# Optimization experiments

Hardware: AMD Instinct MI355X
Metric: run time of the kernel (lower is better)

The kernel has to match this reference:

```python
import jax, jax.numpy as jnp
import numpy as np

MAX_SH_DEGREE = 3
NUM_BASES = (MAX_SH_DEGREE + 1) ** 2  # 16


def eval_sh_bases_fast(dirs):
    """SH bases up to degree 3 for unit directions [..., 3] -> [..., 16].
    Matches gsplat's _eval_sh_bases_fast constants/order."""
    x, y, z = dirs[..., 0], dirs[..., 1], dirs[..., 2]
    z2 = z * z
    fTmp0B = -1.092548430592079 * z
    fC1 = x * x - y * y
    fS1 = 2.0 * x * y
    fTmp0C = -2.285228997322329 * z2 + 0.4570457994644658
    fTmp1B = 1.445305721320277 * z
    fC2 = x * fC1 - y * fS1
    fS2 = x * fS1 + y * fC1
    ones = jnp.full_like(x, 0.2820947917738781)
    return jnp.stack([
        ones,
        -0.48860251190292 * y,
        0.48860251190292 * z,
        -0.48860251190292 * x,
        0.5462742152960395 * fS1,
        fTmp0B * y,
        0.9461746957575601 * z2 - 0.3153915652525201,
        fTmp0B * x,
        0.5462742152960395 * fC1,
        -0.5900435899266435 * fS2,
        fTmp1B * fS1,
        fTmp0C * y,
        z * (1.865881662950577 * z2 - 1.119528997770346),
        fTmp0C * x,
        fTmp1B * fC1,
        -0.5900435899266435 * fC2,
    ], axis=-1)


def setup_inputs() -> dict:
    key = jax.random.key(0)
    ks = jax.random.split(key, 10)
    C, N, F, E, W = 4, 250000, 32, 16, 128
    D_IN = E + F + NUM_BASES  # 64
    return {
        "features": jax.random.normal(ks[0], (N, F), jnp.float32),
        "dirs": jax.random.normal(ks[1], (C, N, 3), jnp.float32),
        "embed_table": jax.random.normal(ks[2], (1000, E), jnp.float32) * 0.1,
        "W0": jax.random.normal(ks[3], (D_IN, W), jnp.float32) / np.sqrt(D_IN),
        "b0": jax.random.normal(ks[4], (W,), jnp.float32) * 0.01,
        "W1": jax.random.normal(ks[5], (W, W), jnp.float32) / np.sqrt(W),
        "b1": jax.random.normal(ks[6], (W,), jnp.float32) * 0.01,
        "W2": jax.random.normal(ks[7], (W, 3), jnp.float32) / np.sqrt(W),
        "b2": jax.random.normal(ks[8], (3,), jnp.float32) * 0.01,
        "embed_ids": jax.random.randint(ks[9], (C,), 0, 1000, jnp.int64 if jax.config.jax_enable_x64 else jnp.int32),
        "sh_degree": 3,
    }


def reference(features, dirs, embed_table, W0, b0, W1, b1, W2, b2, embed_ids, sh_degree):
    C, N = dirs.shape[:2]
    E = embed_table.shape[1]
    F_dim = features.shape[1]
    # camera embeddings broadcast over splats
    emb = embed_table[embed_ids]                                   # [C, E]
    emb = jnp.broadcast_to(emb[:, None, :], (C, N, E))
    feats = jnp.broadcast_to(features[None, :, :], (C, N, F_dim))
    # F.normalize(dirs, dim=-1): divide by norm clamped at eps=1e-12
    norm = jnp.linalg.norm(dirs, axis=-1, keepdims=True)
    nd = dirs / jnp.maximum(norm, 1e-12)
    nb_use = (sh_degree + 1) ** 2  # static python int
    sh = eval_sh_bases_fast(nd)                                    # [C, N, 16]
    if nb_use < NUM_BASES:  # zero bases beyond requested degree
        mask = (jnp.arange(NUM_BASES) < nb_use).astype(sh.dtype)
        sh = sh * mask
    x = jnp.concatenate([emb, feats, sh], axis=-1)                 # [C, N, 64]
    h = jax.nn.relu(x @ W0 + b0)
    h = jax.nn.relu(h @ W1 + b1)
    return h @ W2 + b2                                             # [C, N, 3]
```

## Files before the change

### kernel.cpp

```cpp
#include <hip/hip_runtime.h>
#include <cstdint>
#include <cstddef>

typedef _Float16 half8 __attribute__((ext_vector_type(8)));
typedef __fp16 fp16x2 __attribute__((ext_vector_type(2)));
typedef float floatx16 __attribute__((ext_vector_type(16)));


__global__ void vdc_prep_kernel(const float* __restrict__ W0,
                                const float* __restrict__ W1,
                                const float* __restrict__ W2,
                                const float* __restrict__ b0,
                                const float* __restrict__ b1,
                                const float* __restrict__ b2,
                                const float* __restrict__ emb_tab,
                                const int* __restrict__ embed_ids,
                                int C,
                                _Float16* __restrict__ ws) {
    int i = blockIdx.x * 256 + threadIdx.x;
    int w0end = C * 8192;
    int w1end = w0end + 18432;
    int w2end = w1end + 4608;
    float v = 0.0f;
    if (i < w0end) {
        int c = i >> 13, r = i & 8191;
        int ci = r >> 9, l = (r >> 3) & 63, ii = r & 7;
        int mt = ci >> 2, ks = ci & 3;
        int j  = mt * 32 + (l & 31);
        int kk = ks * 16 + (l >> 5) * 8 + ii;
        if (kk < 48) v = W0[(16 + kk) * 128 + j];
        else if (kk == 48) {
            int id = embed_ids[c];
            v = b0[j];
            #pragma unroll
            for (int e = 0; e < 16; ++e)
                v += emb_tab[(size_t)id * 16 + e] * W0[e * 128 + j];
        }
        ws[i] = (_Float16)v;
    } else if (i < w1end) {
        int r = i - w0end;
        int ci = r >> 9, l = (r >> 3) & 63, ii = r & 7;
        int mt = ci / 9, ks = ci - mt * 9;
        int j  = mt * 32 + (l & 31);
        int kk = ks * 16 + (l >> 5) * 8 + ii;
        if (kk < 128) v = W1[kk * 128 + j];
        else if (kk == 128) v = b1[j];
        ws[i] = (_Float16)v;
    } else if (i < w2end) {
        int r = i - w1end;
        int ks = r >> 9, l = (r >> 3) & 63, ii = r & 7;
        int o  = l & 31;
        int kk = ks * 16 + (l >> 5) * 8 + ii;
        if (o < 3) {
            if (kk < 128) v = W2[kk * 3 + o];
            else if (kk == 128) v = b2[o];
        }
        ws[i] = (_Float16)v;
    }
}

union U4 { unsigned u[4]; half8 h; };

__device__ __forceinline__ unsigned pkr(float a, float b) {
    union { fp16x2 h; unsigned u; } x;
    x.h = __builtin_amdgcn_cvt_pkrtz(a, b);
    return x.u;
}

__device__ __forceinline__ void transition(const floatx16& a, int hl,
                                           half8& lo, half8& hi) {
    unsigned p0 = pkr(fmaxf(a[0],  0.f), fmaxf(a[1],  0.f));
    unsigned p1 = pkr(fmaxf(a[2],  0.f), fmaxf(a[3],  0.f));
    unsigned p2 = pkr(fmaxf(a[4],  0.f), fmaxf(a[5],  0.f));
    unsigned p3 = pkr(fmaxf(a[6],  0.f), fmaxf(a[7],  0.f));
    unsigned p4 = pkr(fmaxf(a[8],  0.f), fmaxf(a[9],  0.f));
    unsigned p5 = pkr(fmaxf(a[10], 0.f), fmaxf(a[11], 0.f));
    unsigned p6 = pkr(fmaxf(a[12], 0.f), fmaxf(a[13], 0.f));
    unsigned p7 = pkr(fmaxf(a[14], 0.f), fmaxf(a[15], 0.f));
    unsigned r0 = __shfl_xor(hl ? p0 : p2, 32);
    unsigned r1 = __shfl_xor(hl ? p1 : p3, 32);
    unsigned r2 = __shfl_xor(hl ? p4 : p6, 32);
    unsigned r3 = __shfl_xor(hl ? p5 : p7, 32);
    U4 L, H;
    L.u[0] = hl ? r0 : p0;
    L.u[1] = hl ? r1 : p1;
    L.u[2] = hl ? p2 : r0;
    L.u[3] = hl ? p3 : r1;
    H.u[0] = hl ? r2 : p4;
    H.u[1] = hl ? r3 : p5;
    H.u[2] = hl ? p6 : r2;
    H.u[3] = hl ? p7 : r3;
    lo = L.h; hi = H.h;
}

#define MFMA(a, b, c) __builtin_amdgcn_mfma_f32_32x32x16_f16((a), (b), (c), 0, 0, 0)

__global__ __launch_bounds__(512, 2) void vdc_mlp_kernel(
    const float* __restrict__ feats,
    const float* __restrict__ dirs,
    const int* __restrict__ sh_deg_p,
    const _Float16* __restrict__ ws,
    float* __restrict__ out,
    int N, int C)
{
    __shared__ uint4 arena[3904];
    char* lds = (char*)arena;

    const int tid   = threadIdx.x;
    const int c     = blockIdx.y;
    const int w     = tid >> 6;
    const int lane  = tid & 63;
    const int ln    = lane & 31;
    const int hl    = lane >> 5;
    const int base0 = blockIdx.x * 512 + w * 64;

    {
        const uint4* srcA = (const uint4*)(ws + (size_t)c * 8192);
        const uint4* srcB = (const uint4*)(ws + (size_t)C * 8192);
        #pragma unroll
        for (int it = 0; it < 8; ++it) {
            int idx = it * 512 + tid;
            if (idx < 3904)
                arena[idx] = (idx < 1024) ? srcA[idx] : srcB[idx - 1024];
        }
    }

    half8 bx0[2], bx1[2], bx2[2], bbias;
    {
        U4 ub;
        ub.u[0] = hl ? 0u : 0x00003C00u;
        ub.u[1] = 0u; ub.u[2] = 0u; ub.u[3] = 0u;
        bbias = ub.h;
    }
    int deg = sh_deg_p[0];
    int nbu = (deg + 1) * (deg + 1);
    #pragma unroll
    for (int b = 0; b < 2; ++b) {
        int n = base0 + b * 32 + ln; if (n >= N) n = N - 1;
        const float* fp = feats + (size_t)n * 32 + hl * 8;
        float4 f0 = *(const float4*)(fp);
        float4 f1 = *(const float4*)(fp + 4);
        float4 f2 = *(const float4*)(fp + 16);
        float4 f3 = *(const float4*)(fp + 20);
        U4 u0, u1;
        u0.u[0] = pkr(f0.x, f0.y); u0.u[1] = pkr(f0.z, f0.w);
        u0.u[2] = pkr(f1.x, f1.y); u0.u[3] = pkr(f1.z, f1.w);
        u1.u[0] = pkr(f2.x, f2.y); u1.u[1] = pkr(f2.z, f2.w);
        u1.u[2] = pkr(f3.x, f3.y); u1.u[3] = pkr(f3.z, f3.w);
        bx0[b] = u0.h; bx1[b] = u1.h;

        const float* dp = dirs + ((size_t)c * N + n) * 3;
        float dx = dp[0], dy = dp[1], dz = dp[2];
        float nrm = sqrtf(dx * dx + dy * dy + dz * dz);
        float inv = 1.0f / fmaxf(nrm, 1e-12f);
        float x = dx * inv, y = dy * inv, z = dz * inv;

        float z2     = z * z;
        float fTmp0B = -1.092548430592079f * z;
        float fC1    = x * x - y * y;
        float fS1    = 2.0f * x * y;
        float fTmp0C = -2.285228997322329f * z2 + 0.4570457994644658f;
        float fTmp1B = 1.445305721320277f * z;
        float fC2    = x * fC1 - y * fS1;
        float fS2    = x * fS1 + y * fC1;

        float sh[16];
        sh[0]  = 0.2820947917738781f;
        sh[1]  = -0.48860251190292f * y;
        sh[2]  = 0.48860251190292f * z;
        sh[3]  = -0.48860251190292f * x;
        sh[4]  = 0.5462742152960395f * fS1;
        sh[5]  = fTmp0B * y;
        sh[6]  = 0.9461746957575601f * z2 - 0.3153915652525201f;
        sh[7]  = fTmp0B * x;
        sh[8]  = 0.5462742152960395f * fC1;
        sh[9]  = -0.5900435899266435f * fS2;
        sh[10] = fTmp1B * fS1;
        sh[11] = fTmp0C * y;
        sh[12] = z * (1.865881662950577f * z2 - 1.119528997770346f);
        sh[13] = fTmp0C * x;
        sh[14] = fTmp1B * fC1;
        sh[15] = -0.5900435899266435f * fC2;
        #pragma unroll
        for (int i = 0; i < 16; ++i) if (i >= nbu) sh[i] = 0.0f;

        float s[8];
        #pragma unroll
        for (int i = 0; i < 8; ++i) s[i] = hl ? sh[8 + i] : sh[i];
        U4 u2;
        u2.u[0] = pkr(s[0], s[1]); u2.u[1] = pkr(s[2], s[3]);
        u2.u[2] = pkr(s[4], s[5]); u2.u[3] = pkr(s[6], s[7]);
        bx2[b] = u2.h;
    }

    __syncthreads();

    const char* fr = lds + lane * 16;

    half8 hx[2][8];
    #pragma unroll
    for (int mt = 0; mt < 4; ++mt) {
        half8 a0 = *(const half8*)(fr + (mt * 4 + 0) * 1024);
        half8 a1 = *(const half8*)(fr + (mt * 4 + 1) * 1024);
        half8 a2 = *(const half8*)(fr + (mt * 4 + 2) * 1024);
        half8 a3 = *(const half8*)(fr + (mt * 4 + 3) * 1024);
        #pragma unroll
        for (int b = 0; b < 2; ++b) {
            floatx16 acc;
            #pragma unroll
            for (int r = 0; r < 16; ++r) acc[r] = 0.0f;
            acc = MFMA(a0, bx0[b], acc);
            acc = MFMA(a1, bx1[b], acc);
            acc = MFMA(a2, bx2[b], acc);
            acc = MFMA(a3, bbias, acc);
            transition(acc, hl, hx[b][2 * mt], hx[b][2 * mt + 1]);
        }
    }

    half8 gx[2][8];
    #pragma unroll
    for (int mt = 0; mt < 4; ++mt) {
        const char* ap = fr + 16384 + mt * 9 * 1024;
        #pragma unroll
        for (int b = 0; b < 2; ++b) {
            floatx16 acc;
            #pragma unroll
            for (int r = 0; r < 16; ++r) acc[r] = 0.0f;
            #pragma unroll
            for (int ks = 0; ks < 8; ++ks) {
                half8 a = *(const half8*)(ap + ks * 1024);
                acc = MFMA(a, hx[b][ks], acc);
            }
            half8 ab = *(const half8*)(ap + 8 * 1024);
            acc = MFMA(ab, bbias, acc);
            transition(acc, hl, gx[b][2 * mt], gx[b][2 * mt + 1]);
        }
    }

    #pragma unroll
    for (int b = 0; b < 2; ++b) {
        floatx16 acc;
        #pragma unroll
        for (int r = 0; r < 16; ++r) acc[r] = 0.0f;
        const char* ap = fr + 53248;
        #pragma unroll
        for (int ks = 0; ks < 8; ++ks) {
            half8 a = *(const half8*)(ap + ks * 1024);
            acc = MFMA(a, gx[b][ks], acc);
        }
        half8 ab = *(const half8*)(ap + 8 * 1024);
        acc = MFMA(ab, bbias, acc);

        if (hl == 0) {
            int nn = base0 + b * 32 + ln;
            if (nn < N) {
                float* op = out + ((size_t)c * N + nn) * 3;
                op[0] = acc[0];
                op[1] = acc[1];
                op[2] = acc[2];
            }
        }
    }
}

extern "C" void kernel_launch(void* const* d_in, const int* in_sizes, int n_in,
                              void* d_out, int out_size, void* d_ws, size_t ws_size,
                              hipStream_t stream) {
    const float* feats   = (const float*)d_in[0];
    const float* dirs    = (const float*)d_in[1];
    const float* emb_tab = (const float*)d_in[2];
    const float* W0      = (const float*)d_in[3];
    const float* b0      = (const float*)d_in[4];
    const float* W1      = (const float*)d_in[5];
    const float* b1      = (const float*)d_in[6];
    const float* W2      = (const float*)d_in[7];
    const float* b2      = (const float*)d_in[8];
    const int*   eids    = (const int*)d_in[9];
    const int*   shd     = (const int*)d_in[10];
    float* outp          = (float*)d_out;

    int N = in_sizes[0] / 32;
    int C = in_sizes[9];

    _Float16* wsh = (_Float16*)d_ws;

    int ws_elems = C * 8192 + 23040;
    vdc_prep_kernel<<<(ws_elems + 255) / 256, 256, 0, stream>>>(
        W0, W1, W2, b0, b1, b2, emb_tab, eids, C, wsh);

    dim3 grid((N + 511) / 512, C);
    vdc_mlp_kernel<<<grid, 512, 0, stream>>>(
        feats, dirs, shd, wsh, outp, N, C);
}
```

Before: 183.4 us.

## Fuse weight preparation into MLP kernel and halve points per block

```diff
diff --git a/kernel.cpp b/kernel.cpp
--- a/kernel.cpp
+++ b/kernel.cpp
@@ -6,58 +6,6 @@
 typedef __fp16 fp16x2 __attribute__((ext_vector_type(2)));
 typedef float floatx16 __attribute__((ext_vector_type(16)));
 
-
-__global__ void vdc_prep_kernel(const float* __restrict__ W0,
-                                const float* __restrict__ W1,
-                                const float* __restrict__ W2,
-                                const float* __restrict__ b0,
-                                const float* __restrict__ b1,
-                                const float* __restrict__ b2,
-                                const float* __restrict__ emb_tab,
-                                const int* __restrict__ embed_ids,
-                                int C,
-                                _Float16* __restrict__ ws) {
-    int i = blockIdx.x * 256 + threadIdx.x;
-    int w0end = C * 8192;
-    int w1end = w0end + 18432;
-    int w2end = w1end + 4608;
-    float v = 0.0f;
-    if (i < w0end) {
-        int c = i >> 13, r = i & 8191;
-        int ci = r >> 9, l = (r >> 3) & 63, ii = r & 7;
-        int mt = ci >> 2, ks = ci & 3;
-        int j  = mt * 32 + (l & 31);
-        int kk = ks * 16 + (l >> 5) * 8 + ii;
-        if (kk < 48) v = W0[(16 + kk) * 128 + j];
-        else if (kk == 48) {
-            int id = embed_ids[c];
-            v = b0[j];
-            #pragma unroll
-            for (int e = 0; e < 16; ++e)
-                v += emb_tab[(size_t)id * 16 + e] * W0[e * 128 + j];
-        }
-        ws[i] = (_Float16)v;
-    } else if (i < w1end) {
-        int r = i - w0end;
-        int ci = r >> 9, l = (r >> 3) & 63, ii = r & 7;
-        int mt = ci / 9, ks = ci - mt * 9;
-        int j  = mt * 32 + (l & 31);
-        int kk = ks * 16 + (l >> 5) * 8 + ii;
-        if (kk < 128) v = W1[kk * 128 + j];
-        else if (kk == 128) v = b1[j];
-        ws[i] = (_Float16)v;
-    } else if (i < w2end) {
-        int r = i - w1end;
-        int ks = r >> 9, l = (r >> 3) & 63, ii = r & 7;
-        int o  = l & 31;
-        int kk = ks * 16 + (l >> 5) * 8 + ii;
-        if (o < 3) {
-            if (kk < 128) v = W2[kk * 3 + o];
-            else if (kk == 128) v = b2[o];
-        }
-        ws[i] = (_Float16)v;
-    }
-}
 
 union U4 { unsigned u[4]; half8 h; };
 
@@ -95,13 +43,20 @@
 
 #define MFMA(a, b, c) __builtin_amdgcn_mfma_f32_32x32x16_f16((a), (b), (c), 0, 0, 0)
 
-__global__ __launch_bounds__(512, 2) void vdc_mlp_kernel(
+__global__ __launch_bounds__(512, 4) void vdc_mlp_kernel(
     const float* __restrict__ feats,
     const float* __restrict__ dirs,
+    const float* __restrict__ emb_tab,
+    const float* __restrict__ W0,
+    const float* __restrict__ b0,
+    const float* __restrict__ W1,
+    const float* __restrict__ b1,
+    const float* __restrict__ W2,
+    const float* __restrict__ b2,
+    const int* __restrict__ embed_ids,
     const int* __restrict__ sh_deg_p,
-    const _Float16* __restrict__ ws,
     float* __restrict__ out,
-    int N, int C)
+    int N)
 {
     __shared__ uint4 arena[3904];
     char* lds = (char*)arena;
@@ -112,31 +67,77 @@
     const int lane  = tid & 63;
     const int ln    = lane & 31;
     const int hl    = lane >> 5;
-    const int base0 = blockIdx.x * 512 + w * 64;
-
-    {
-        const uint4* srcA = (const uint4*)(ws + (size_t)c * 8192);
-        const uint4* srcB = (const uint4*)(ws + (size_t)C * 8192);
-        #pragma unroll
-        for (int it = 0; it < 8; ++it) {
-            int idx = it * 512 + tid;
-            if (idx < 3904)
-                arena[idx] = (idx < 1024) ? srcA[idx] : srcB[idx - 1024];
-        }
-    }
-
-    half8 bx0[2], bx1[2], bx2[2], bbias;
+    const int base  = blockIdx.x * 256 + w * 32;
+
+    #pragma unroll
+    for (int q = 0; q < 8; ++q) {
+        int idx = q * 512 + tid;
+        if (idx < 3904) arena[idx] = uint4{0, 0, 0, 0};
+    }
+    __syncthreads();
+
+    #pragma unroll
+    for (int q = 0; q < 8; ++q) {
+        int fidx = q * 512 + tid;
+        int k   = fidx >> 5;
+        int j4  = (fidx & 31) * 4;
+        float4 v = *(const float4*)(W1 + k * 128 + j4);
+        int ks = k >> 4;
+        int lv = 32 * ((k >> 3) & 1);
+        int by = (k & 7) * 2;
+        float vv[4] = {v.x, v.y, v.z, v.w};
+        #pragma unroll
+        for (int d = 0; d < 4; ++d) {
+            int j = j4 + d;
+            char* p = lds + 16384 + ((j >> 5) * 9 + ks) * 1024 + ((j & 31) + lv) * 16 + by;
+            *(_Float16*)p = (_Float16)vv[d];
+        }
+    }
+    #pragma unroll
+    for (int q = 0; q < 3; ++q) {
+        int fidx = q * 512 + tid;
+        int kk  = fidx >> 5;
+        int j4  = (fidx & 31) * 4;
+        float4 v = *(const float4*)(W0 + (16 + kk) * 128 + j4);
+        int ks = kk >> 4;
+        int lv = 32 * ((kk >> 3) & 1);
+        int by = (kk & 7) * 2;
+        float vv[4] = {v.x, v.y, v.z, v.w};
+        #pragma unroll
+        for (int d = 0; d < 4; ++d) {
+            int j = j4 + d;
+            char* p = lds + ((j >> 5) * 4 + ks) * 1024 + ((j & 31) + lv) * 16 + by;
+            *(_Float16*)p = (_Float16)vv[d];
+        }
+    }
+    if (tid < 128) {
+        int j = tid;
+        int id = embed_ids[c];
+        float a = b0[j];
+        #pragma unroll
+        for (int e = 0; e < 16; ++e)
+            a += emb_tab[(size_t)id * 16 + e] * W0[e * 128 + j];
+        *(_Float16*)(lds + ((j >> 5) * 4 + 3) * 1024 + (j & 31) * 16) = (_Float16)a;
+        *(_Float16*)(lds + 16384 + ((j >> 5) * 9 + 8) * 1024 + (j & 31) * 16) = (_Float16)b1[j];
+    } else if (tid < 512 && tid >= 128 && tid < 128 + 384) {
+        int t = tid - 128;
+        int k = t / 3, o = t - 3 * k;
+        float v = W2[k * 3 + o];
+        char* p = lds + 53248 + (k >> 4) * 1024 + (o + 32 * ((k >> 3) & 1)) * 16 + (k & 7) * 2;
+        *(_Float16*)p = (_Float16)v;
+    }
+    if (tid < 3)
+        *(_Float16*)(lds + 53248 + 8 * 1024 + tid * 16) = (_Float16)b2[tid];
+
+    half8 bx0, bx1, bx2, bbias;
     {
         U4 ub;
         ub.u[0] = hl ? 0u : 0x00003C00u;
         ub.u[1] = 0u; ub.u[2] = 0u; ub.u[3] = 0u;
         bbias = ub.h;
     }
-    int deg = sh_deg_p[0];
-    int nbu = (deg + 1) * (deg + 1);
-    #pragma unroll
-    for (int b = 0; b < 2; ++b) {
-        int n = base0 + b * 32 + ln; if (n >= N) n = N - 1;
+    {
+        int n = base + ln; if (n >= N) n = N - 1;
         const float* fp = feats + (size_t)n * 32 + hl * 8;
         float4 f0 = *(const float4*)(fp);
         float4 f1 = *(const float4*)(fp + 4);
@@ -147,7 +148,7 @@
         u0.u[2] = pkr(f1.x, f1.y); u0.u[3] = pkr(f1.z, f1.w);
         u1.u[0] = pkr(f2.x, f2.y); u1.u[1] = pkr(f2.z, f2.w);
         u1.u[2] = pkr(f3.x, f3.y); u1.u[3] = pkr(f3.z, f3.w);
-        bx0[b] = u0.h; bx1[b] = u1.h;
+        bx0 = u0.h; bx1 = u1.h;
 
         const float* dp = dirs + ((size_t)c * N + n) * 3;
         float dx = dp[0], dy = dp[1], dz = dp[2];
@@ -181,6 +182,9 @@
         sh[13] = fTmp0C * x;
         sh[14] = fTmp1B * fC1;
         sh[15] = -0.5900435899266435f * fC2;
+
+        int deg = sh_deg_p[0];
+        int nbu = (deg + 1) * (deg + 1);
         #pragma unroll
         for (int i = 0; i < 16; ++i) if (i >= nbu) sh[i] = 0.0f;
 
@@ -190,55 +194,48 @@
         U4 u2;
         u2.u[0] = pkr(s[0], s[1]); u2.u[1] = pkr(s[2], s[3]);
         u2.u[2] = pkr(s[4], s[5]); u2.u[3] = pkr(s[6], s[7]);
-        bx2[b] = u2.h;
+        bx2 = u2.h;
     }
 
     __syncthreads();
 
     const char* fr = lds + lane * 16;
 
-    half8 hx[2][8];
+    half8 hx[8];
     #pragma unroll
     for (int mt = 0; mt < 4; ++mt) {
         half8 a0 = *(const half8*)(fr + (mt * 4 + 0) * 1024);
         half8 a1 = *(const half8*)(fr + (mt * 4 + 1) * 1024);
         half8 a2 = *(const half8*)(fr + (mt * 4 + 2) * 1024);
         half8 a3 = *(const half8*)(fr + (mt * 4 + 3) * 1024);
-        #pragma unroll
-        for (int b = 0; b < 2; ++b) {
-            floatx16 acc;
-            #pragma unroll
-            for (int r = 0; r < 16; ++r) acc[r] = 0.0f;
-            acc = MFMA(a0, bx0[b], acc);
-            acc = MFMA(a1, bx1[b], acc);
-            acc = MFMA(a2, bx2[b], acc);
-            acc = MFMA(a3, bbias, acc);
-            transition(acc, hl, hx[b][2 * mt], hx[b][2 * mt + 1]);
-        }
-    }
-
-    half8 gx[2][8];
+        floatx16 acc;
+        #pragma unroll
+        for (int r = 0; r < 16; ++r) acc[r] = 0.0f;
+        acc = MFMA(a0, bx0, acc);
+        acc = MFMA(a1, bx1, acc);
+        acc = MFMA(a2, bx2, acc);
+        acc = MFMA(a3, bbias, acc);
+        transition(acc, hl, hx[2 * mt], hx[2 * mt + 1]);
+    }
+
+    half8 gx[8];
     #pragma unroll
     for (int mt = 0; mt < 4; ++mt) {
         const char* ap = fr + 16384 + mt * 9 * 1024;
-        #pragma unroll
-        for (int b = 0; b < 2; ++b) {
-            floatx16 acc;
-            #pragma unroll
-            for (int r = 0; r < 16; ++r) acc[r] = 0.0f;
-            #pragma unroll
-            for (int ks = 0; ks < 8; ++ks) {
-                half8 a = *(const half8*)(ap + ks * 1024);
-                acc = MFMA(a, hx[b][ks], acc);
-            }
-            half8 ab = *(const half8*)(ap + 8 * 1024);
-            acc = MFMA(ab, bbias, acc);
-            transition(acc, hl, gx[b][2 * mt], gx[b][2 * mt + 1]);
-        }
-    }
-
-    #pragma unroll
-    for (int b = 0; b < 2; ++b) {
+        floatx16 acc;
+        #pragma unroll
+        for (int r = 0; r < 16; ++r) acc[r] = 0.0f;
+        #pragma unroll
+        for (int ks = 0; ks < 8; ++ks) {
+            half8 a = *(const half8*)(ap + ks * 1024);
+            acc = MFMA(a, hx[ks], acc);
+        }
+        half8 ab = *(const half8*)(ap + 8 * 1024);
+        acc = MFMA(ab, bbias, acc);
+        transition(acc, hl, gx[2 * mt], gx[2 * mt + 1]);
+    }
+
+    {
         floatx16 acc;
         #pragma unroll
         for (int r = 0; r < 16; ++r) acc[r] = 0.0f;
@@ -246,13 +243,13 @@
         #pragma unroll
         for (int ks = 0; ks < 8; ++ks) {
             half8 a = *(const half8*)(ap + ks * 1024);
-            acc = MFMA(a, gx[b][ks], acc);
+            acc = MFMA(a, gx[ks], acc);
         }
         half8 ab = *(const half8*)(ap + 8 * 1024);
         acc = MFMA(ab, bbias, acc);
 
         if (hl == 0) {
-            int nn = base0 + b * 32 + ln;
+            int nn = base + ln;
             if (nn < N) {
                 float* op = out + ((size_t)c * N + nn) * 3;
                 op[0] = acc[0];
@@ -282,13 +279,7 @@
     int N = in_sizes[0] / 32;
     int C = in_sizes[9];
 
-    _Float16* wsh = (_Float16*)d_ws;
-
-    int ws_elems = C * 8192 + 23040;
-    vdc_prep_kernel<<<(ws_elems + 255) / 256, 256, 0, stream>>>(
-        W0, W1, W2, b0, b1, b2, emb_tab, eids, C, wsh);
-
-    dim3 grid((N + 511) / 512, C);
+    dim3 grid((N + 255) / 256, C);
     vdc_mlp_kernel<<<grid, 512, 0, stream>>>(
-        feats, dirs, shd, wsh, outp, N, C);
-}
+        feats, dirs, emb_tab, W0, b0, W1, b1, W2, b2, eids, shd, outp, N);
+}
```

Result: slower. 219.5 us (+19.7%).

## Halve per-wave batch and stream layer-3 MFMAs to raise occupancy

Applied to the files above, without the earlier changes.

```diff
diff --git a/kernel.cpp b/kernel.cpp
--- a/kernel.cpp
+++ b/kernel.cpp
@@ -95,7 +95,7 @@
 
 #define MFMA(a, b, c) __builtin_amdgcn_mfma_f32_32x32x16_f16((a), (b), (c), 0, 0, 0)
 
-__global__ __launch_bounds__(512, 2) void vdc_mlp_kernel(
+__global__ __launch_bounds__(512, 4) void vdc_mlp_kernel(
     const float* __restrict__ feats,
     const float* __restrict__ dirs,
     const int* __restrict__ sh_deg_p,
@@ -112,7 +112,7 @@
     const int lane  = tid & 63;
     const int ln    = lane & 31;
     const int hl    = lane >> 5;
-    const int base0 = blockIdx.x * 512 + w * 64;
+    const int base  = blockIdx.x * 256 + w * 32;
 
     {
         const uint4* srcA = (const uint4*)(ws + (size_t)c * 8192);
@@ -125,18 +125,15 @@
         }
     }
 
-    half8 bx0[2], bx1[2], bx2[2], bbias;
+    half8 bx0, bx1, bx2, bbias;
     {
         U4 ub;
         ub.u[0] = hl ? 0u : 0x00003C00u;
         ub.u[1] = 0u; ub.u[2] = 0u; ub.u[3] = 0u;
         bbias = ub.h;
     }
-    int deg = sh_deg_p[0];
-    int nbu = (deg + 1) * (deg + 1);
-    #pragma unroll
-    for (int b = 0; b < 2; ++b) {
-        int n = base0 + b * 32 + ln; if (n >= N) n = N - 1;
+    {
+        int n = base + ln; if (n >= N) n = N - 1;
         const float* fp = feats + (size_t)n * 32 + hl * 8;
         float4 f0 = *(const float4*)(fp);
         float4 f1 = *(const float4*)(fp + 4);
@@ -147,7 +144,7 @@
         u0.u[2] = pkr(f1.x, f1.y); u0.u[3] = pkr(f1.z, f1.w);
         u1.u[0] = pkr(f2.x, f2.y); u1.u[1] = pkr(f2.z, f2.w);
         u1.u[2] = pkr(f3.x, f3.y); u1.u[3] = pkr(f3.z, f3.w);
-        bx0[b] = u0.h; bx1[b] = u1.h;
+        bx0 = u0.h; bx1 = u1.h;
 
         const float* dp = dirs + ((size_t)c * N + n) * 3;
         float dx = dp[0], dy = dp[1], dz = dp[2];
@@ -181,6 +178,9 @@
         sh[13] = fTmp0C * x;
         sh[14] = fTmp1B * fC1;
         sh[15] = -0.5900435899266435f * fC2;
+
+        int deg = sh_deg_p[0];
+        int nbu = (deg + 1) * (deg + 1);
         #pragma unroll
         for (int i = 0; i < 16; ++i) if (i >= nbu) sh[i] = 0.0f;
 
@@ -190,75 +190,68 @@
         U4 u2;
         u2.u[0] = pkr(s[0], s[1]); u2.u[1] = pkr(s[2], s[3]);
         u2.u[2] = pkr(s[4], s[5]); u2.u[3] = pkr(s[6], s[7]);
-        bx2[b] = u2.h;
+        bx2 = u2.h;
     }
 
     __syncthreads();
 
     const char* fr = lds + lane * 16;
 
-    half8 hx[2][8];
+    half8 hx[8];
     #pragma unroll
     for (int mt = 0; mt < 4; ++mt) {
         half8 a0 = *(const half8*)(fr + (mt * 4 + 0) * 1024);
         half8 a1 = *(const half8*)(fr + (mt * 4 + 1) * 1024);
         half8 a2 = *(const half8*)(fr + (mt * 4 + 2) * 1024);
         half8 a3 = *(const half8*)(fr + (mt * 4 + 3) * 1024);
-        #pragma unroll
-        for (int b = 0; b < 2; ++b) {
-            floatx16 acc;
-            #pragma unroll
-            for (int r = 0; r < 16; ++r) acc[r] = 0.0f;
-            acc = MFMA(a0, bx0[b], acc);
-            acc = MFMA(a1, bx1[b], acc);
-            acc = MFMA(a2, bx2[b], acc);
-            acc = MFMA(a3, bbias, acc);
-            transition(acc, hl, hx[b][2 * mt], hx[b][2 * mt + 1]);
-        }
-    }
-
-    half8 gx[2][8];
+        floatx16 acc;
+        #pragma unroll
+        for (int r = 0; r < 16; ++r) acc[r] = 0.0f;
+        acc = MFMA(a0, bx0, acc);
+        acc = MFMA(a1, bx1, acc);
+        acc = MFMA(a2, bx2, acc);
+        acc = MFMA(a3, bbias, acc);
+        transition(acc, hl, hx[2 * mt], hx[2 * mt + 1]);
+    }
+
+    floatx16 acc3;
+    #pragma unroll
+    for (int r = 0; r < 16; ++r) acc3[r] = 0.0f;
+
     #pragma unroll
     for (int mt = 0; mt < 4; ++mt) {
         const char* ap = fr + 16384 + mt * 9 * 1024;
-        #pragma unroll
-        for (int b = 0; b < 2; ++b) {
-            floatx16 acc;
-            #pragma unroll
-            for (int r = 0; r < 16; ++r) acc[r] = 0.0f;
-            #pragma unroll
-            for (int ks = 0; ks < 8; ++ks) {
-                half8 a = *(const half8*)(ap + ks * 1024);
-                acc = MFMA(a, hx[b][ks], acc);
-            }
-            half8 ab = *(const half8*)(ap + 8 * 1024);
-            acc = MFMA(ab, bbias, acc);
-            transition(acc, hl, gx[b][2 * mt], gx[b][2 * mt + 1]);
-        }
-    }
-
-    #pragma unroll
-    for (int b = 0; b < 2; ++b) {
         floatx16 acc;
         #pragma unroll
         for (int r = 0; r < 16; ++r) acc[r] = 0.0f;
-        const char* ap = fr + 53248;
         #pragma unroll
         for (int ks = 0; ks < 8; ++ks) {
             half8 a = *(const half8*)(ap + ks * 1024);
-            acc = MFMA(a, gx[b][ks], acc);
+            acc = MFMA(a, hx[ks], acc);
         }
         half8 ab = *(const half8*)(ap + 8 * 1024);
         acc = MFMA(ab, bbias, acc);
 
-        if (hl == 0) {
-            int nn = base0 + b * 32 + ln;
-            if (nn < N) {
-                float* op = out + ((size_t)c * N + nn) * 3;
-                op[0] = acc[0];
-                op[1] = acc[1];
-                op[2] = acc[2];
-            }
+        half8 g0, g1;
+        transition(acc, hl, g0, g1);
+
+        half8 w2a = *(const half8*)(fr + 53248 + (2 * mt + 0) * 1024);
+        half8 w2b = *(const half8*)(fr + 53248 + (2 * mt + 1) * 1024);
+        acc3 = MFMA(w2a, g0, acc3);
+        acc3 = MFMA(w2b, g1, acc3);
+    }
+    {
+        half8 ab = *(const half8*)(fr + 53248 + 8 * 1024);
+        acc3 = MFMA(ab, bbias, acc3);
+    }
+
+    if (hl == 0) {
+        int nn = base + ln;
+        if (nn < N) {
+            float* op = out + ((size_t)c * N + nn) * 3;
+            op[0] = acc3[0];
+            op[1] = acc3[1];
+            op[2] = acc3[2];
         }
     }
 }
@@ -288,7 +281,7 @@
     vdc_prep_kernel<<<(ws_elems + 255) / 256, 256, 0, stream>>>(
         W0, W1, W2, b0, b1, b2, emb_tab, eids, C, wsh);
 
-    dim3 grid((N + 511) / 512, C);
+    dim3 grid((N + 255) / 256, C);
     vdc_mlp_kernel<<<grid, 512, 0, stream>>>(
         feats, dirs, shd, wsh, outp, N, C);
 }
```

Result: faster. 165.0 us (-10.0%).

## Halve block size and fuse layer-3 MFMA into layer-2 loop to cut registers

Applied to the files above, without the earlier changes.

```diff
diff --git a/kernel.cpp b/kernel.cpp
--- a/kernel.cpp
+++ b/kernel.cpp
@@ -95,7 +95,7 @@
 
 #define MFMA(a, b, c) __builtin_amdgcn_mfma_f32_32x32x16_f16((a), (b), (c), 0, 0, 0)
 
-__global__ __launch_bounds__(512, 2) void vdc_mlp_kernel(
+__global__ __launch_bounds__(256, 2) void vdc_mlp_kernel(
     const float* __restrict__ feats,
     const float* __restrict__ dirs,
     const int* __restrict__ sh_deg_p,
@@ -112,17 +112,18 @@
     const int lane  = tid & 63;
     const int ln    = lane & 31;
     const int hl    = lane >> 5;
-    const int base0 = blockIdx.x * 512 + w * 64;
+    const int base  = blockIdx.x * 256 + w * 64;
 
     {
         const uint4* srcA = (const uint4*)(ws + (size_t)c * 8192);
         const uint4* srcB = (const uint4*)(ws + (size_t)C * 8192);
         #pragma unroll
-        for (int it = 0; it < 8; ++it) {
-            int idx = it * 512 + tid;
-            if (idx < 3904)
-                arena[idx] = (idx < 1024) ? srcA[idx] : srcB[idx - 1024];
-        }
+        for (int it = 0; it < 15; ++it) {
+            int idx = it * 256 + tid;
+            arena[idx] = (idx < 1024) ? srcA[idx] : srcB[idx - 1024];
+        }
+        int idx = 15 * 256 + tid;
+        if (idx < 3904) arena[idx] = srcB[idx - 1024];
     }
 
     half8 bx0[2], bx1[2], bx2[2], bbias;
@@ -136,7 +137,7 @@
     int nbu = (deg + 1) * (deg + 1);
     #pragma unroll
     for (int b = 0; b < 2; ++b) {
-        int n = base0 + b * 32 + ln; if (n >= N) n = N - 1;
+        int n = base + b * 32 + ln; if (n >= N) n = N - 1;
         const float* fp = feats + (size_t)n * 32 + hl * 8;
         float4 f0 = *(const float4*)(fp);
         float4 f1 = *(const float4*)(fp + 4);
@@ -217,10 +218,17 @@
         }
     }
 
-    half8 gx[2][8];
+    floatx16 acc3[2];
+    #pragma unroll
+    for (int b = 0; b < 2; ++b)
+        #pragma unroll
+        for (int r = 0; r < 16; ++r) acc3[b][r] = 0.0f;
+
     #pragma unroll
     for (int mt = 0; mt < 4; ++mt) {
         const char* ap = fr + 16384 + mt * 9 * 1024;
+        half8 w2a = *(const half8*)(fr + 53248 + (2 * mt + 0) * 1024);
+        half8 w2b = *(const half8*)(fr + 53248 + (2 * mt + 1) * 1024);
         #pragma unroll
         for (int b = 0; b < 2; ++b) {
             floatx16 acc;
@@ -233,31 +241,29 @@
             }
             half8 ab = *(const half8*)(ap + 8 * 1024);
             acc = MFMA(ab, bbias, acc);
-            transition(acc, hl, gx[b][2 * mt], gx[b][2 * mt + 1]);
-        }
-    }
-
-    #pragma unroll
-    for (int b = 0; b < 2; ++b) {
-        floatx16 acc;
-        #pragma unroll
-        for (int r = 0; r < 16; ++r) acc[r] = 0.0f;
-        const char* ap = fr + 53248;
-        #pragma unroll
-        for (int ks = 0; ks < 8; ++ks) {
-            half8 a = *(const half8*)(ap + ks * 1024);
-            acc = MFMA(a, gx[b][ks], acc);
-        }
-        half8 ab = *(const half8*)(ap + 8 * 1024);
-        acc = MFMA(ab, bbias, acc);
-
-        if (hl == 0) {
-            int nn = base0 + b * 32 + ln;
+
+            half8 g0, g1;
+            transition(acc, hl, g0, g1);
+            acc3[b] = MFMA(w2a, g0, acc3[b]);
+            acc3[b] = MFMA(w2b, g1, acc3[b]);
+        }
+    }
+    {
+        half8 ab = *(const half8*)(fr + 53248 + 8 * 1024);
+        #pragma unroll
+        for (int b = 0; b < 2; ++b)
+            acc3[b] = MFMA(ab, bbias, acc3[b]);
+    }
+
+    if (hl == 0) {
+        #pragma unroll
+        for (int b = 0; b < 2; ++b) {
+            int nn = base + b * 32 + ln;
             if (nn < N) {
                 float* op = out + ((size_t)c * N + nn) * 3;
-                op[0] = acc[0];
-                op[1] = acc[1];
-                op[2] = acc[2];
+                op[0] = acc3[b][0];
+                op[1] = acc3[b][1];
+                op[2] = acc3[b][2];
             }
         }
     }
@@ -288,7 +294,7 @@
     vdc_prep_kernel<<<(ws_elems + 255) / 256, 256, 0, stream>>>(
         W0, W1, W2, b0, b1, b2, emb_tab, eids, C, wsh);
 
-    dim3 grid((N + 511) / 512, C);
-    vdc_mlp_kernel<<<grid, 512, 0, stream>>>(
+    dim3 grid((N + 255) / 256, C);
+    vdc_mlp_kernel<<<grid, 256, 0, stream>>>(
         feats, dirs, shd, wsh, outp, N, C);
 }
```

New measurement: 194.4 us. 1.06x slower.
